# Kernel tuning notes

Hardware: AMD Instinct MI355X
Metric: run time of the kernel (lower is better)

## Reference

```python
import jax, jax.numpy as jnp
import numpy as np

BETA = 0.5

def setup_inputs() -> dict:
    key = jax.random.key(0)
    ks = jax.random.split(key, 10)
    B, H = 4096, 200
    ITEM, REGION = 100000, 1000
    D, HID = 128, 64  # embed_size, hidden_size
    half = D // 2
    history = jax.random.randint(ks[0], (B, H), 0, ITEM)
    target = jax.random.randint(ks[1], (B,), 0, ITEM)
    history_region = jax.random.randint(ks[2], (B, H), 0, REGION)
    target_region = jax.random.randint(ks[3], (B,), 0, REGION)
    W_hist = jax.random.normal(ks[4], (ITEM, half), jnp.float32) * 0.01
    W_tgt = jax.random.normal(ks[5], (ITEM, half), jnp.float32) * 0.01
    W_reg = jax.random.normal(ks[6], (REGION, half), jnp.float32) * 0.01
    W1 = jax.random.normal(ks[7], (D, HID), jnp.float32) * (1.0 / np.sqrt(D))
    b1 = jnp.zeros((HID,), jnp.float32)
    W2 = jax.random.normal(ks[8], (HID,), jnp.float32) * (1.0 / np.sqrt(HID))
    return {"history": history, "target": target,
            "history_region": history_region, "target_region": target_region,
            "W_hist": W_hist, "W_tgt": W_tgt, "W_reg": W_reg,
            "W1": W1, "b1": b1, "W2": W2}

def reference(history, target, history_region, target_region,
              W_hist, W_tgt, W_reg, W1, b1, W2):
    # gather + concat: [B,H,D] and [B,D]
    h = jnp.concatenate([W_hist[history], W_reg[history_region]], axis=-1)
    t = jnp.concatenate([W_tgt[target], W_reg[target_region]], axis=-1)
    inp = h * t[:, None, :]                      # [B,H,D]
    r1 = jax.nn.relu(inp @ W1 + b1)              # [B,H,HID] (dropout = identity at eval)
    logits = r1 @ W2                             # [B,H]
    mask = (history != target[:, None]).astype(logits.dtype)
    exp_A = jnp.exp(logits) * mask               # [B,H]
    exp_sum = jnp.sum(exp_A, axis=-1) ** BETA    # [B], beta-power normalization
    attn = exp_A / exp_sum[:, None]              # [B,H]
    pred = jnp.einsum('bhd,bd->b', h * attn[..., None], t)
    return jax.nn.sigmoid(pred)
```

## Files before the change

kernel.cpp:

```cpp
#include <hip/hip_runtime.h>
#include <math.h>

#define NB        4096
#define NH        200
#define HIST_ROWS 100000
#define REG_ROWS  1000
#define NTILES    13

typedef __attribute__((ext_vector_type(4))) int   int4i;

#define SA 2048.0f
#define SB 16384.0f
#define ST 2048.0f
#define INV_LOGIT (1.0f / (SA * SB))
#define INV_S     (1.0f / (SA * ST))

__device__ __forceinline__ int q8(float x, float s) {
    return __float2int_rn(fminf(fmaxf(x * s, -127.f), 127.f));
}
__device__ __forceinline__ int pack4(float a, float b, float c, float d, float s) {
    const int x0 = q8(a, s), x1 = q8(b, s), x2 = q8(c, s), x3 = q8(d, s);
    return (x0 & 255) | ((x1 & 255) << 8) | ((x2 & 255) << 16) | (x3 << 24);
}

__global__ __launch_bounds__(256) void prep_i8(
    const float* __restrict__ Wh, const float* __restrict__ Wr,
    const float* __restrict__ W1,
    unsigned char* __restrict__ tab, float* __restrict__ W1F2)
{
    for (int i = blockIdx.x * blockDim.x + threadIdx.x; i < 10240;
         i += gridDim.x * blockDim.x) {
        const int chunk = i >> 4, j = i & 15;
        const int frag = chunk >> 6, nt = frag >> 1, ks = frag & 1;
        const int c = chunk & 63, q = c >> 4, l = c & 15;
        W1F2[i] = (nt < 4) ? W1[(ks * 64 + q * 16 + j) * 64 + nt * 16 + l] : 0.f;
    }
    const int total = (HIST_ROWS + REG_ROWS) * 16;
    const int HE    = HIST_ROWS * 16;
    unsigned* dst = (unsigned*)tab;
    for (int i = blockIdx.x * blockDim.x + threadIdx.x; i < total;
         i += gridDim.x * blockDim.x) {
        const float4 v = (i < HE) ? ((const float4*)Wh)[i]
                                  : ((const float4*)Wr)[i - HE];
        dst[i] = (unsigned)pack4(v.x, v.y, v.z, v.w, SA);
    }
}

__device__ __forceinline__ void epi_store_i8(
    const int4i* accT, const float* w2v, const float* b1v,
    int tl, int quad, int l15, float* logit_lds, float* s_lds)
{
    float part[4] = {0.f, 0.f, 0.f, 0.f};
    #pragma unroll
    for (int nt = 0; nt < 4; ++nt)
        #pragma unroll
        for (int r = 0; r < 4; ++r)
            part[r] += fmaxf((float)accT[nt][r] * INV_LOGIT + b1v[nt], 0.f) * w2v[nt];
    #pragma unroll
    for (int r = 0; r < 4; ++r) {
        part[r] += __shfl_xor(part[r], 1);
        part[r] += __shfl_xor(part[r], 2);
        part[r] += __shfl_xor(part[r], 4);
        part[r] += __shfl_xor(part[r], 8);
    }
    if (l15 == 0) {
        const int jg = tl * 16 + quad * 4;
        #pragma unroll
        for (int r = 0; r < 4; ++r) {
            logit_lds[jg + r] = part[r];
            s_lds[jg + r]     = (float)accT[4][r] * INV_S;
        }
    }
}

__device__ __forceinline__ int4i quant_row_fp32(const float* row, int quad) {
    const float4* p = (const float4*)(row + quad * 16);
    const float4 v0 = p[0], v1 = p[1], v2 = p[2], v3 = p[3];
    int4i o;
    o.x = pack4(v0.x, v0.y, v0.z, v0.w, SA);
    o.y = pack4(v1.x, v1.y, v1.z, v1.w, SA);
    o.z = pack4(v2.x, v2.y, v2.z, v2.w, SA);
    o.w = pack4(v3.x, v3.y, v3.z, v3.w, SA);
    return o;
}

template <bool BT>
__global__ __launch_bounds__(256, 4) void nais_i8(
    const int*   __restrict__ history,
    const int*   __restrict__ target,
    const int*   __restrict__ history_region,
    const int*   __restrict__ target_region,
    const float* __restrict__ W_hist,
    const float* __restrict__ W_tgt,
    const float* __restrict__ W_reg,
    const float* __restrict__ W1,
    const float* __restrict__ b1,
    const float* __restrict__ W2,
    const unsigned char* __restrict__ tab,
    const float* __restrict__ W1F2,
    float*       __restrict__ out)
{
    __shared__ int hist_lds[224];
    __shared__ int hreg_lds[224];
    __shared__ __align__(16) int Bf4[640 * 4];
    __shared__ float logit_lds[208];
    __shared__ float s_lds[208];
    __shared__ float red_e[4], red_p[4];

    const int b   = blockIdx.x;
    const int tid = threadIdx.x;
    const int lane = tid & 63, wv = tid >> 6;
    const int l15  = lane & 15, quad = lane >> 4;

    const int  tls[4] = {wv, wv + 4, wv + 8, wv + 12};
    const bool has3   = (tls[3] < NTILES);

    const int tgt  = target[b];
    const int treg = target_region[b];

    int4i A[4][2];
    if (BT) {
        int ih[4], ir[4];
        #pragma unroll
        for (int tt = 0; tt < 4; ++tt) {
            int j = ((tt == 3 && !has3) ? tls[2] : tls[tt]) * 16 + l15;
            if (j >= NH) j = NH - 1;
            ih[tt] = history[b * NH + j];
            ir[tt] = history_region[b * NH + j];
        }
        #pragma unroll
        for (int tt = 0; tt < 4; ++tt) {
            A[tt][0] = *(const int4i*)(tab + (size_t)ih[tt] * 64 + quad * 16);
            A[tt][1] = *(const int4i*)(tab + (size_t)(HIST_ROWS + ir[tt]) * 64 + quad * 16);
        }
    }

    if (BT) {
        if (tid < NH) hist_lds[tid] = history[b * NH + tid];
    } else {
        if (tid < 224) {
            const int jj = tid < NH ? tid : NH - 1;
            hist_lds[tid] = history[b * NH + jj];
            hreg_lds[tid] = history_region[b * NH + jj];
        }
    }

    float w2v[4], b1v[4];
    #pragma unroll
    for (int nt = 0; nt < 4; ++nt) {
        w2v[nt] = W2[nt * 16 + l15];
        b1v[nt] = b1[nt * 16 + l15];
    }

    const float* tW = W_tgt + (size_t)tgt * 64;
    const float* rW = W_reg + (size_t)treg * 64;

    #pragma unroll
    for (int v = 0; v < 3; ++v) {
        const int i = tid + v * 256;
        if (i < 640) {
            const int frag = i >> 6, nt = frag >> 1, ks = frag & 1;
            const int c = i & 63, q = c >> 4, l = c & 15;
            const float4* tp = (const float4*)((ks == 0) ? (tW + q * 16)
                                                         : (rW + q * 16));
            const float4 t0 = tp[0], t1 = tp[1], t2 = tp[2], t3 = tp[3];
            int4i ob;
            if (nt < 4) {
                float4 w0, w1, w2, w3;
                if (BT) {
                    const float4* wp = (const float4*)(W1F2 + i * 16);
                    w0 = wp[0]; w1 = wp[1]; w2 = wp[2]; w3 = wp[3];
                } else {
                    const int n = nt * 16 + l;
                    const int k0 = ks * 64 + q * 16;
                    float tmp[16];
                    #pragma unroll
                    for (int j = 0; j < 16; ++j) tmp[j] = W1[(k0 + j) * 64 + n];
                    w0 = make_float4(tmp[0], tmp[1], tmp[2], tmp[3]);
                    w1 = make_float4(tmp[4], tmp[5], tmp[6], tmp[7]);
                    w2 = make_float4(tmp[8], tmp[9], tmp[10], tmp[11]);
                    w3 = make_float4(tmp[12], tmp[13], tmp[14], tmp[15]);
                }
                ob.x = pack4(w0.x * t0.x, w0.y * t0.y, w0.z * t0.z, w0.w * t0.w, SB);
                ob.y = pack4(w1.x * t1.x, w1.y * t1.y, w1.z * t1.z, w1.w * t1.w, SB);
                ob.z = pack4(w2.x * t2.x, w2.y * t2.y, w2.z * t2.z, w2.w * t2.w, SB);
                ob.w = pack4(w3.x * t3.x, w3.y * t3.y, w3.z * t3.z, w3.w * t3.w, SB);
            } else {
                if (l == 0) {
                    ob.x = pack4(t0.x, t0.y, t0.z, t0.w, ST);
                    ob.y = pack4(t1.x, t1.y, t1.z, t1.w, ST);
                    ob.z = pack4(t2.x, t2.y, t2.z, t2.w, ST);
                    ob.w = pack4(t3.x, t3.y, t3.z, t3.w, ST);
                } else {
                    ob = (int4i){0, 0, 0, 0};
                }
            }
            *reinterpret_cast<int4i*>(&Bf4[i * 4]) = ob;
        }
    }
    __syncthreads();

    #pragma unroll
    for (int pp = 0; pp < 2; ++pp) {
        const int t0i = pp * 2, t1i = pp * 2 + 1;
        const bool hb = (t1i < 3) || has3;

        if (!BT) {
            #pragma unroll
            for (int tt = 0; tt < 2; ++tt) {
                const int ti = t0i + tt;
                const int j  = ((ti == 3 && !has3) ? tls[2] : tls[ti]) * 16 + l15;
                A[ti][0] = quant_row_fp32(W_hist + (size_t)hist_lds[j] * 64, quad);
                A[ti][1] = quant_row_fp32(W_reg  + (size_t)hreg_lds[j] * 64, quad);
            }
        }

        int4i acc[2][5];
        #pragma unroll
        for (int tt = 0; tt < 2; ++tt)
            #pragma unroll
            for (int nt = 0; nt < 5; ++nt) acc[tt][nt] = (int4i){0, 0, 0, 0};

        #pragma unroll
        for (int ks = 0; ks < 2; ++ks) {
            int4i bf[5];
            #pragma unroll
            for (int nt = 0; nt < 5; ++nt)
                bf[nt] = *reinterpret_cast<const int4i*>(&Bf4[((nt * 2 + ks) * 64 + lane) * 4]);
            #pragma unroll
            for (int nt = 0; nt < 5; ++nt)
                acc[0][nt] = __builtin_amdgcn_mfma_i32_16x16x64_i8(A[t0i][ks], bf[nt], acc[0][nt], 0, 0, 0);
            if (hb) {
                #pragma unroll
                for (int nt = 0; nt < 5; ++nt)
                    acc[1][nt] = __builtin_amdgcn_mfma_i32_16x16x64_i8(A[t1i][ks], bf[nt], acc[1][nt], 0, 0, 0);
            }
        }

        epi_store_i8(acc[0], w2v, b1v, tls[t0i], quad, l15, logit_lds, s_lds);
        if (hb) epi_store_i8(acc[1], w2v, b1v, tls[t1i], quad, l15, logit_lds, s_lds);
    }
    __syncthreads();

    float e = 0.f, p = 0.f;
    if (tid < NH) {
        const float ex = (hist_lds[tid] != tgt) ? expf(logit_lds[tid]) : 0.f;
        e = ex;
        p = ex * s_lds[tid];
    }
    #pragma unroll
    for (int off = 32; off > 0; off >>= 1) {
        e += __shfl_down(e, off);
        p += __shfl_down(p, off);
    }
    if (lane == 0) { red_e[wv] = e; red_p[wv] = p; }
    __syncthreads();
    if (tid == 0) {
        const float E = red_e[0] + red_e[1] + red_e[2] + red_e[3];
        const float P = red_p[0] + red_p[1] + red_p[2] + red_p[3];
        const float pred = P / sqrtf(E);
        out[b] = 1.f / (1.f + expf(-pred));
    }
}

extern "C" void kernel_launch(void* const* d_in, const int* in_sizes, int n_in,
                              void* d_out, int out_size, void* d_ws, size_t ws_size,
                              hipStream_t stream) {
    const int*   history        = (const int*)  d_in[0];
    const int*   target         = (const int*)  d_in[1];
    const int*   history_region = (const int*)  d_in[2];
    const int*   target_region  = (const int*)  d_in[3];
    const float* W_hist         = (const float*)d_in[4];
    const float* W_tgt          = (const float*)d_in[5];
    const float* W_reg          = (const float*)d_in[6];
    const float* W1             = (const float*)d_in[7];
    const float* b1             = (const float*)d_in[8];
    const float* W2             = (const float*)d_in[9];
    float* out = (float*)d_out;

    const size_t tab_bytes = (size_t)(HIST_ROWS + REG_ROWS) * 64;
    const size_t need = tab_bytes + 10240 * 4;
    if (ws_size >= need) {
        unsigned char* tab = (unsigned char*)d_ws;
        float* W1F2 = (float*)((char*)d_ws + tab_bytes);
        prep_i8<<<2048, 256, 0, stream>>>(W_hist, W_reg, W1, tab, W1F2);
        nais_i8<true><<<NB, 256, 0, stream>>>(history, target, history_region, target_region,
                                              W_hist, W_tgt, W_reg, W1, b1, W2, tab, W1F2, out);
    } else {
        nais_i8<false><<<NB, 256, 0, stream>>>(history, target, history_region, target_region,
                                               W_hist, W_tgt, W_reg, W1, b1, W2, nullptr, nullptr, out);
    }
}
```

Before: 138.8 us.

## Drop int8 table prep kernel; gather fp32 rows directly with prefetch overlap

Removes the separate prep kernel that quantized the whole 100k-row embedding table and transposed W1 into a workspace each call. The main kernel now gathers fp32 history and region rows directly and quantizes them in registers. It prefetches the first two tiles before the B-fragment build and the last two after it. This avoids a full-table pass per call, but each gathered row is now 256 bytes instead of 64, and the kernel holds more registers, so launch bounds drop to 3 blocks.

```diff
diff --git a/kernel.cpp b/kernel.cpp
--- a/kernel.cpp
+++ b/kernel.cpp
@@ -23,59 +23,8 @@
     return (x0 & 255) | ((x1 & 255) << 8) | ((x2 & 255) << 16) | (x3 << 24);
 }
 
-__global__ __launch_bounds__(256) void prep_i8(
-    const float* __restrict__ Wh, const float* __restrict__ Wr,
-    const float* __restrict__ W1,
-    unsigned char* __restrict__ tab, float* __restrict__ W1F2)
-{
-    for (int i = blockIdx.x * blockDim.x + threadIdx.x; i < 10240;
-         i += gridDim.x * blockDim.x) {
-        const int chunk = i >> 4, j = i & 15;
-        const int frag = chunk >> 6, nt = frag >> 1, ks = frag & 1;
-        const int c = chunk & 63, q = c >> 4, l = c & 15;
-        W1F2[i] = (nt < 4) ? W1[(ks * 64 + q * 16 + j) * 64 + nt * 16 + l] : 0.f;
-    }
-    const int total = (HIST_ROWS + REG_ROWS) * 16;
-    const int HE    = HIST_ROWS * 16;
-    unsigned* dst = (unsigned*)tab;
-    for (int i = blockIdx.x * blockDim.x + threadIdx.x; i < total;
-         i += gridDim.x * blockDim.x) {
-        const float4 v = (i < HE) ? ((const float4*)Wh)[i]
-                                  : ((const float4*)Wr)[i - HE];
-        dst[i] = (unsigned)pack4(v.x, v.y, v.z, v.w, SA);
-    }
-}
-
-__device__ __forceinline__ void epi_store_i8(
-    const int4i* accT, const float* w2v, const float* b1v,
-    int tl, int quad, int l15, float* logit_lds, float* s_lds)
-{
-    float part[4] = {0.f, 0.f, 0.f, 0.f};
-    #pragma unroll
-    for (int nt = 0; nt < 4; ++nt)
-        #pragma unroll
-        for (int r = 0; r < 4; ++r)
-            part[r] += fmaxf((float)accT[nt][r] * INV_LOGIT + b1v[nt], 0.f) * w2v[nt];
-    #pragma unroll
-    for (int r = 0; r < 4; ++r) {
-        part[r] += __shfl_xor(part[r], 1);
-        part[r] += __shfl_xor(part[r], 2);
-        part[r] += __shfl_xor(part[r], 4);
-        part[r] += __shfl_xor(part[r], 8);
-    }
-    if (l15 == 0) {
-        const int jg = tl * 16 + quad * 4;
-        #pragma unroll
-        for (int r = 0; r < 4; ++r) {
-            logit_lds[jg + r] = part[r];
-            s_lds[jg + r]     = (float)accT[4][r] * INV_S;
-        }
-    }
-}
-
-__device__ __forceinline__ int4i quant_row_fp32(const float* row, int quad) {
-    const float4* p = (const float4*)(row + quad * 16);
-    const float4 v0 = p[0], v1 = p[1], v2 = p[2], v3 = p[3];
+__device__ __forceinline__ int4i quant16(const float4& v0, const float4& v1,
+                                         const float4& v2, const float4& v3) {
     int4i o;
     o.x = pack4(v0.x, v0.y, v0.z, v0.w, SA);
     o.y = pack4(v1.x, v1.y, v1.z, v1.w, SA);
@@ -84,8 +33,34 @@
     return o;
 }
 
-template <bool BT>
-__global__ __launch_bounds__(256, 4) void nais_i8(
+__device__ __forceinline__ void epi_store_i8(
+    const int4i* accT, const float* w2v, const float* b1v,
+    int tl, int quad, int l15, float* logit_lds, float* s_lds)
+{
+    float part[4] = {0.f, 0.f, 0.f, 0.f};
+    #pragma unroll
+    for (int nt = 0; nt < 4; ++nt)
+        #pragma unroll
+        for (int r = 0; r < 4; ++r)
+            part[r] += fmaxf((float)accT[nt][r] * INV_LOGIT + b1v[nt], 0.f) * w2v[nt];
+    #pragma unroll
+    for (int r = 0; r < 4; ++r) {
+        part[r] += __shfl_xor(part[r], 1);
+        part[r] += __shfl_xor(part[r], 2);
+        part[r] += __shfl_xor(part[r], 4);
+        part[r] += __shfl_xor(part[r], 8);
+    }
+    if (l15 == 0) {
+        const int jg = tl * 16 + quad * 4;
+        #pragma unroll
+        for (int r = 0; r < 4; ++r) {
+            logit_lds[jg + r] = part[r];
+            s_lds[jg + r]     = (float)accT[4][r] * INV_S;
+        }
+    }
+}
+
+__global__ __launch_bounds__(256, 3) void nais_nw(
     const int*   __restrict__ history,
     const int*   __restrict__ target,
     const int*   __restrict__ history_region,
@@ -96,12 +71,9 @@
     const float* __restrict__ W1,
     const float* __restrict__ b1,
     const float* __restrict__ W2,
-    const unsigned char* __restrict__ tab,
-    const float* __restrict__ W1F2,
     float*       __restrict__ out)
 {
     __shared__ int hist_lds[224];
-    __shared__ int hreg_lds[224];
     __shared__ __align__(16) int Bf4[640 * 4];
     __shared__ float logit_lds[208];
     __shared__ float s_lds[208];
@@ -118,31 +90,29 @@
     const int tgt  = target[b];
     const int treg = target_region[b];
 
-    int4i A[4][2];
-    if (BT) {
-        int ih[4], ir[4];
-        #pragma unroll
-        for (int tt = 0; tt < 4; ++tt) {
-            int j = ((tt == 3 && !has3) ? tls[2] : tls[tt]) * 16 + l15;
-            if (j >= NH) j = NH - 1;
-            ih[tt] = history[b * NH + j];
-            ir[tt] = history_region[b * NH + j];
-        }
-        #pragma unroll
-        for (int tt = 0; tt < 4; ++tt) {
-            A[tt][0] = *(const int4i*)(tab + (size_t)ih[tt] * 64 + quad * 16);
-            A[tt][1] = *(const int4i*)(tab + (size_t)(HIST_ROWS + ir[tt]) * 64 + quad * 16);
-        }
-    }
-
-    if (BT) {
-        if (tid < NH) hist_lds[tid] = history[b * NH + tid];
-    } else {
-        if (tid < 224) {
-            const int jj = tid < NH ? tid : NH - 1;
-            hist_lds[tid] = history[b * NH + jj];
-            hreg_lds[tid] = history_region[b * NH + jj];
-        }
+    int ihx[4], irx[4];
+    #pragma unroll
+    for (int tt = 0; tt < 4; ++tt) {
+        int j = ((tt == 3 && !has3) ? tls[2] : tls[tt]) * 16 + l15;
+        if (j >= NH) j = NH - 1;
+        ihx[tt] = history[b * NH + j];
+        irx[tt] = history_region[b * NH + j];
+    }
+
+    float4 F[2][2][4];
+    #pragma unroll
+    for (int tt = 0; tt < 2; ++tt) {
+        const float4* ph = (const float4*)(W_hist + (size_t)ihx[tt] * 64 + quad * 16);
+        const float4* pr = (const float4*)(W_reg  + (size_t)irx[tt] * 64 + quad * 16);
+        #pragma unroll
+        for (int s = 0; s < 4; ++s) F[tt][0][s] = ph[s];
+        #pragma unroll
+        for (int s = 0; s < 4; ++s) F[tt][1][s] = pr[s];
+    }
+
+    if (tid < 224) {
+        const int jj = tid < NH ? tid : NH - 1;
+        hist_lds[tid] = history[b * NH + jj];
     }
 
     float w2v[4], b1v[4];
@@ -161,30 +131,19 @@
         if (i < 640) {
             const int frag = i >> 6, nt = frag >> 1, ks = frag & 1;
             const int c = i & 63, q = c >> 4, l = c & 15;
-            const float4* tp = (const float4*)((ks == 0) ? (tW + q * 16)
-                                                         : (rW + q * 16));
+            const float4* tp = (const float4*)(((ks == 0) ? tW : rW) + q * 16);
             const float4 t0 = tp[0], t1 = tp[1], t2 = tp[2], t3 = tp[3];
             int4i ob;
             if (nt < 4) {
-                float4 w0, w1, w2, w3;
-                if (BT) {
-                    const float4* wp = (const float4*)(W1F2 + i * 16);
-                    w0 = wp[0]; w1 = wp[1]; w2 = wp[2]; w3 = wp[3];
-                } else {
-                    const int n = nt * 16 + l;
-                    const int k0 = ks * 64 + q * 16;
-                    float tmp[16];
-                    #pragma unroll
-                    for (int j = 0; j < 16; ++j) tmp[j] = W1[(k0 + j) * 64 + n];
-                    w0 = make_float4(tmp[0], tmp[1], tmp[2], tmp[3]);
-                    w1 = make_float4(tmp[4], tmp[5], tmp[6], tmp[7]);
-                    w2 = make_float4(tmp[8], tmp[9], tmp[10], tmp[11]);
-                    w3 = make_float4(tmp[12], tmp[13], tmp[14], tmp[15]);
-                }
-                ob.x = pack4(w0.x * t0.x, w0.y * t0.y, w0.z * t0.z, w0.w * t0.w, SB);
-                ob.y = pack4(w1.x * t1.x, w1.y * t1.y, w1.z * t1.z, w1.w * t1.w, SB);
-                ob.z = pack4(w2.x * t2.x, w2.y * t2.y, w2.z * t2.z, w2.w * t2.w, SB);
-                ob.w = pack4(w3.x * t3.x, w3.y * t3.y, w3.z * t3.z, w3.w * t3.w, SB);
+                const int n  = nt * 16 + l;
+                const int k0 = ks * 64 + q * 16;
+                float tmp[16];
+                #pragma unroll
+                for (int j = 0; j < 16; ++j) tmp[j] = W1[(k0 + j) * 64 + n];
+                ob.x = pack4(tmp[0]  * t0.x, tmp[1]  * t0.y, tmp[2]  * t0.z, tmp[3]  * t0.w, SB);
+                ob.y = pack4(tmp[4]  * t1.x, tmp[5]  * t1.y, tmp[6]  * t1.z, tmp[7]  * t1.w, SB);
+                ob.z = pack4(tmp[8]  * t2.x, tmp[9]  * t2.y, tmp[10] * t2.z, tmp[11] * t2.w, SB);
+                ob.w = pack4(tmp[12] * t3.x, tmp[13] * t3.y, tmp[14] * t3.z, tmp[15] * t3.w, SB);
             } else {
                 if (l == 0) {
                     ob.x = pack4(t0.x, t0.y, t0.z, t0.w, ST);
@@ -200,18 +159,32 @@
     }
     __syncthreads();
 
+    int4i A[4][2];
+    #pragma unroll
+    for (int tt = 0; tt < 2; ++tt) {
+        A[tt][0] = quant16(F[tt][0][0], F[tt][0][1], F[tt][0][2], F[tt][0][3]);
+        A[tt][1] = quant16(F[tt][1][0], F[tt][1][1], F[tt][1][2], F[tt][1][3]);
+    }
+    #pragma unroll
+    for (int tt = 2; tt < 4; ++tt) {
+        const float4* ph = (const float4*)(W_hist + (size_t)ihx[tt] * 64 + quad * 16);
+        const float4* pr = (const float4*)(W_reg  + (size_t)irx[tt] * 64 + quad * 16);
+        #pragma unroll
+        for (int s = 0; s < 4; ++s) F[tt - 2][0][s] = ph[s];
+        #pragma unroll
+        for (int s = 0; s < 4; ++s) F[tt - 2][1][s] = pr[s];
+    }
+
     #pragma unroll
     for (int pp = 0; pp < 2; ++pp) {
         const int t0i = pp * 2, t1i = pp * 2 + 1;
         const bool hb = (t1i < 3) || has3;
 
-        if (!BT) {
-            #pragma unroll
-            for (int tt = 0; tt < 2; ++tt) {
-                const int ti = t0i + tt;
-                const int j  = ((ti == 3 && !has3) ? tls[2] : tls[ti]) * 16 + l15;
-                A[ti][0] = quant_row_fp32(W_hist + (size_t)hist_lds[j] * 64, quad);
-                A[ti][1] = quant_row_fp32(W_reg  + (size_t)hreg_lds[j] * 64, quad);
+        if (pp == 1) {
+            #pragma unroll
+            for (int tt = 2; tt < 4; ++tt) {
+                A[tt][0] = quant16(F[tt - 2][0][0], F[tt - 2][0][1], F[tt - 2][0][2], F[tt - 2][0][3]);
+                A[tt][1] = quant16(F[tt - 2][1][0], F[tt - 2][1][1], F[tt - 2][1][2], F[tt - 2][1][3]);
             }
         }
 
@@ -278,16 +251,8 @@
     const float* W2             = (const float*)d_in[9];
     float* out = (float*)d_out;
 
-    const size_t tab_bytes = (size_t)(HIST_ROWS + REG_ROWS) * 64;
-    const size_t need = tab_bytes + 10240 * 4;
-    if (ws_size >= need) {
-        unsigned char* tab = (unsigned char*)d_ws;
-        float* W1F2 = (float*)((char*)d_ws + tab_bytes);
-        prep_i8<<<2048, 256, 0, stream>>>(W_hist, W_reg, W1, tab, W1F2);
-        nais_i8<true><<<NB, 256, 0, stream>>>(history, target, history_region, target_region,
-                                              W_hist, W_tgt, W_reg, W1, b1, W2, tab, W1F2, out);
-    } else {
-        nais_i8<false><<<NB, 256, 0, stream>>>(history, target, history_region, target_region,
-                                               W_hist, W_tgt, W_reg, W1, b1, W2, nullptr, nullptr, out);
-    }
-}
+    (void)d_ws; (void)ws_size;
+
+    nais_nw<<<NB, 256, 0, stream>>>(history, target, history_region, target_region,
+                                    W_hist, W_tgt, W_reg, W1, b1, W2, out);
+}
```

Measured after the change: 176.0 us. 26.8% more time.
